# Performance work log

Hardware: AMD Instinct MI355X
Metric: run time of the kernel (lower is better)

Reference implementation:

```python
import jax, jax.numpy as jnp
import numpy as np

B = 32768; NF = 8; E = 16; V = 100000; D = 4
IN = 2 * NF * E          # 256 = id_dims + agn_dims
FCN = [256, 128, 64]
DIMS = [IN] + FCN
EPS = 1e-5               # BatchNorm1d eps


def setup_inputs() -> dict:
    ks = jax.random.split(jax.random.key(0), 64)
    inp = {
        'id_idx': jax.random.randint(ks[0], (B, NF), 0, V),
        'agn_idx': jax.random.randint(ks[1], (B, NF), 0, V),
        'domain_id': jax.random.randint(ks[2], (B,), 0, D),
        'id_tables': jax.random.normal(ks[3], (NF, V, E), dtype=jnp.float32) * 0.01,
        'agn_tables': jax.random.normal(ks[4], (NF, V, E), dtype=jnp.float32) * 0.01,
    }
    k = 5
    for i in range(len(FCN)):
        din, dout = DIMS[i], DIMS[i + 1]
        inp[f'mlp_W{i}'] = jax.random.normal(ks[k], (D, din, dout), dtype=jnp.float32) / np.sqrt(din).astype(np.float32); k += 1
        inp[f'mlp_b{i}'] = jnp.zeros((D, dout), jnp.float32)
        inp[f'bn_g{i}'] = jnp.ones((D, dout), jnp.float32)
        inp[f'bn_b{i}'] = jnp.zeros((D, dout), jnp.float32)
        inp[f'gate_W1_{i}'] = jax.random.normal(ks[k], (D, IN, dout), dtype=jnp.float32) / np.sqrt(IN).astype(np.float32); k += 1
        inp[f'gate_b1_{i}'] = jnp.zeros((D, dout), jnp.float32)
        inp[f'gate_W2_{i}'] = jax.random.normal(ks[k], (D, dout, dout), dtype=jnp.float32) / np.sqrt(dout).astype(np.float32); k += 1
        inp[f'gate_b2_{i}'] = jnp.zeros((D, dout), jnp.float32)
    inp['fin_W'] = jax.random.normal(ks[k], (D, DIMS[-1], 1), dtype=jnp.float32) / np.sqrt(DIMS[-1]).astype(np.float32)
    inp['fin_b'] = jnp.zeros((D, 1), jnp.float32)
    return inp


def _embed(tables, idx):
    # tables [NF,V,E], idx [B,NF] -> [B, NF*E] (per-feature lookup then concat)
    g = tables[jnp.arange(NF)[None, :], idx]            # [B,NF,E]
    return g.reshape(idx.shape[0], NF * E)


def _ppnet(id_tables, agn_tables, mlp_W, mlp_b, bn_g, bn_b, gW1, gb1, gW2, gb2,
           fin_W, fin_b, id_idx, agn_idx, domain_id):
    id_x = _embed(id_tables, id_idx)                    # [B, 128]
    agn_x = _embed(agn_tables, agn_idx)                 # [B, 128]
    # gate_input = cat(id_x, agn_x.detach())
    gate_in = jnp.concatenate([id_x, jax.lax.stop_gradient(agn_x)], axis=1)  # [B, IN]
    h = None
    for i in range(len(FCN)):
        # GateNU: Linear->ReLU->Linear->2*sigmoid, broadcast over D domain towers
        g1 = jax.nn.relu(jnp.einsum('bi,dio->dbo', gate_in, gW1[i]) + gb1[i][:, None, :])
        gate = 2.0 * jax.nn.sigmoid(jnp.einsum('dbo,dop->dbp', g1, gW2[i]) + gb2[i][:, None, :])
        # MLP layer: Linear -> BatchNorm1d (train-mode batch stats) -> ReLU
        if h is None:
            h = jnp.einsum('bi,dio->dbo', gate_in, mlp_W[i]) + mlp_b[i][:, None, :]
        else:
            h = jnp.einsum('dbi,dio->dbo', h, mlp_W[i]) + mlp_b[i][:, None, :]
        mu = h.mean(axis=1, keepdims=True)
        var = h.var(axis=1, keepdims=True)              # biased, matches torch BN training
        h = (h - mu) * jax.lax.rsqrt(var + EPS) * bn_g[i][:, None, :] + bn_b[i][:, None, :]
        h = jax.nn.relu(h)
        h = h * gate
    out = jax.nn.sigmoid(jnp.einsum('dbh,dho->dbo', h, fin_W) + fin_b[:, None, :])  # [D,B,1]
    out = out[:, :, 0]                                  # [D,B]
    # torch.where masked-select chain == gather the row of the assigned domain
    return out[domain_id, jnp.arange(out.shape[1])]     # [B]


def reference(id_idx, agn_idx, domain_id, id_tables, agn_tables,
              mlp_W0, mlp_b0, bn_g0, bn_b0, gate_W1_0, gate_b1_0, gate_W2_0, gate_b2_0,
              mlp_W1, mlp_b1, bn_g1, bn_b1, gate_W1_1, gate_b1_1, gate_W2_1, gate_b2_1,
              mlp_W2, mlp_b2, bn_g2, bn_b2, gate_W1_2, gate_b1_2, gate_W2_2, gate_b2_2,
              fin_W, fin_b):
    mlp_W = [mlp_W0, mlp_W1, mlp_W2]; mlp_b = [mlp_b0, mlp_b1, mlp_b2]
    bn_g = [bn_g0, bn_g1, bn_g2]; bn_b = [bn_b0, bn_b1, bn_b2]
    gW1 = [gate_W1_0, gate_W1_1, gate_W1_2]; gb1 = [gate_b1_0, gate_b1_1, gate_b1_2]
    gW2 = [gate_W2_0, gate_W2_1, gate_W2_2]; gb2 = [gate_b2_0, gate_b2_1, gate_b2_2]
    return _ppnet(id_tables, agn_tables, mlp_W, mlp_b, bn_g, bn_b, gW1, gb1, gW2, gb2,
                  fin_W, fin_b, id_idx, agn_idx, domain_id)
```

## Files before the change

kernel.cpp:

```cpp
#include <hip/hip_runtime.h>


typedef __attribute__((ext_vector_type(8))) short short8;
typedef __attribute__((ext_vector_type(4))) float floatx4;

#define BATCH 32768
#define NDOM 4
#define TM 128
#define TN 64
#define KSTEP 32
#define LDA 40

__device__ __forceinline__ unsigned short f2b(float f) {
    unsigned u = __float_as_uint(f);
    u += 0x7fffu + ((u >> 16) & 1u);
    return (unsigned short)(u >> 16);
}
__device__ __forceinline__ float b2f(unsigned short h) {
    return __uint_as_float(((unsigned)h) << 16);
}

struct MatDesc { const float* src; unsigned K, N, pfx, total; };
struct PrepArgs { MatDesc m[9]; float* stats; unsigned statsN; unsigned grand; };

__global__ __launch_bounds__(256) void prep_k(PrepArgs a, unsigned short* __restrict__ wt) {
    unsigned e = blockIdx.x * 256 + threadIdx.x;
    if (e < a.statsN) a.stats[e] = 0.f;
    if (e >= a.grand) return;
    int j = 0;
    while (j < 8 && e >= a.m[j].pfx + a.m[j].total) j++;
    const unsigned K = a.m[j].K, N = a.m[j].N;
    const unsigned local = e - a.m[j].pfx;
    const unsigned kn = K * N;
    const unsigned d = local / kn;
    const unsigned r2 = local - d * kn;
    const unsigned n = r2 / K;
    const unsigned k = r2 - n * K;
    wt[e] = f2b(a.m[j].src[((long long)d * K + k) * N + n]);
}

__global__ __launch_bounds__(256) void embed_k(const int* __restrict__ idi, const int* __restrict__ agi,
                                               const float* __restrict__ idt, const float* __restrict__ agt,
                                               unsigned short* __restrict__ gin) {
    int t = blockIdx.x * 256 + threadIdx.x;
    int b = t >> 4, slot = t & 15;
    int f = slot & 7;
    const int* ip = (slot < 8) ? idi : agi;
    const float* tab = (slot < 8) ? idt : agt;
    int ix = ip[b * 8 + f];
    const float* src = tab + ((long long)f * 100000 + ix) * 16;
    unsigned short tmp[16];
#pragma unroll
    for (int j = 0; j < 16; j++) tmp[j] = f2b(src[j]);
    unsigned short* dst = gin + (long long)b * 256 + slot * 16;
    *(uint4*)dst = *(const uint4*)tmp;
    *(uint4*)(dst + 8) = *(const uint4*)(tmp + 8);
}

__global__ __launch_bounds__(256) void gemm_ep(
    const unsigned short* __restrict__ X, long long xds,
    const unsigned short* __restrict__ Wt,
    const float* __restrict__ bias,
    void* outv,
    int N, int K, int mode, int hf32,
    const void* hprev,
    const float* __restrict__ muv, const float* __restrict__ rsv,
    const float* __restrict__ gma, const float* __restrict__ bta,
    float* __restrict__ gsum, float* __restrict__ gssq) {
    __shared__ __align__(16) unsigned short sA[TM * LDA];
    __shared__ __align__(16) unsigned short sB[TN * LDA];
    __shared__ float sSum[TN], sSsq[TN];

    const int t = threadIdx.x;
    const int d = blockIdx.z;
    const int m0 = blockIdx.x * TM, n0 = blockIdx.y * TN;
    const unsigned short* Xp = X + (long long)d * xds + (long long)m0 * K;
    const unsigned short* Wp = Wt + ((long long)d * N + n0) * (long long)K;

    floatx4 acc[2][4];
#pragma unroll
    for (int i = 0; i < 2; i++)
#pragma unroll
        for (int j = 0; j < 4; j++) acc[i][j] = (floatx4)(0.0f);

    const int w = t >> 6, lane = t & 63, lrow = lane & 15, lq = lane >> 4;
    const int arow = t >> 2, ach = t & 3;

    for (int k0 = 0; k0 < K; k0 += KSTEP) {
        *(uint4*)&sA[arow * LDA + ach * 8] = *(const uint4*)&Xp[(long long)arow * K + k0 + ach * 8];
        *(uint4*)&sA[(arow + 64) * LDA + ach * 8] = *(const uint4*)&Xp[(long long)(arow + 64) * K + k0 + ach * 8];
        *(uint4*)&sB[arow * LDA + ach * 8] = *(const uint4*)&Wp[(long long)arow * K + k0 + ach * 8];
        __syncthreads();
        short8 a[2], b[4];
#pragma unroll
        for (int rt = 0; rt < 2; rt++)
            a[rt] = *(const short8*)&sA[(w * 32 + rt * 16 + lrow) * LDA + lq * 8];
#pragma unroll
        for (int ct = 0; ct < 4; ct++)
            b[ct] = *(const short8*)&sB[(ct * 16 + lrow) * LDA + lq * 8];
#pragma unroll
        for (int rt = 0; rt < 2; rt++)
#pragma unroll
            for (int ct = 0; ct < 4; ct++)
                acc[rt][ct] = __builtin_amdgcn_mfma_f32_16x16x32_bf16(a[rt], b[ct], acc[rt][ct], 0, 0, 0);
        __syncthreads();
    }

    if (mode == 0) {
        if (t < TN) { sSum[t] = 0.f; sSsq[t] = 0.f; }
        __syncthreads();
    }

    const long long orow = (long long)d * BATCH + m0;
#pragma unroll
    for (int ct = 0; ct < 4; ct++) {
        const int nl = ct * 16 + lrow;
        const int n = n0 + nl;
        const float bs = bias[d * N + n];
        float mu_ = 0.f, sc_ = 0.f, bb_ = 0.f;
        if (mode == 2) {
            mu_ = muv[d * N + n];
            sc_ = rsv[d * N + n] * gma[d * N + n];
            bb_ = bta[d * N + n];
        }
        float s = 0.f, ss = 0.f;
#pragma unroll
        for (int rt = 0; rt < 2; rt++) {
            const int mb = w * 32 + rt * 16 + lq * 4;
#pragma unroll
            for (int r = 0; r < 4; r++) {
                float v = acc[rt][ct][r] + bs;
                const long long oi = (orow + mb + r) * (long long)N + n;
                if (mode == 0) {
                    s += v; ss += v * v;
                    if (hf32) ((float*)outv)[oi] = v;
                    else ((unsigned short*)outv)[oi] = f2b(v);
                } else if (mode == 1) {
                    v = fmaxf(v, 0.f);
                    ((unsigned short*)outv)[oi] = f2b(v);
                } else {
                    const float gate = 2.f / (1.f + __expf(-v));
                    const float h = hf32 ? ((const float*)hprev)[oi] : b2f(((const unsigned short*)hprev)[oi]);
                    float x = (h - mu_) * sc_ + bb_;
                    x = fmaxf(x, 0.f);
                    ((unsigned short*)outv)[oi] = f2b(x * gate);
                }
            }
        }
        if (mode == 0) {
            s += __shfl_down(s, 32); ss += __shfl_down(ss, 32);
            s += __shfl_down(s, 16); ss += __shfl_down(ss, 16);
            if (lane < 16) {
                atomicAdd(&sSum[nl], s);
                atomicAdd(&sSsq[nl], ss);
            }
        }
    }
    if (mode == 0) {
        __syncthreads();
        if (t < TN) {
            atomicAdd(&gsum[d * N + n0 + t], sSum[t]);
            atomicAdd(&gssq[d * N + n0 + t], sSsq[t]);
        }
    }
}

__global__ void bn_finalize(const float* __restrict__ gsum, const float* __restrict__ gssq,
                            float* __restrict__ muv, float* __restrict__ rsv, int total, float invB) {
    int i = blockIdx.x * blockDim.x + threadIdx.x;
    if (i >= total) return;
    float mu = gsum[i] * invB;
    float var = gssq[i] * invB - mu * mu;
    muv[i] = mu;
    rsv[i] = rsqrtf(var + 1e-5f);
}

__global__ __launch_bounds__(256) void final_k(const unsigned short* __restrict__ X3, const int* __restrict__ dom,
                                               const float* __restrict__ fw, const float* __restrict__ fb,
                                               float* __restrict__ out) {
    int b = blockIdx.x * 256 + threadIdx.x;
    int d = dom[b];
    const unsigned short* x = X3 + ((long long)d * BATCH + b) * 64;
    const float* wp = fw + d * 64;
    float acc = fb[d];
#pragma unroll
    for (int k = 0; k < 64; k++) acc += b2f(x[k]) * wp[k];
    out[b] = 1.f / (1.f + __expf(-acc));
}

extern "C" void kernel_launch(void* const* d_in, const int* in_sizes, int n_in,
                              void* d_out, int out_size, void* d_ws, size_t ws_size,
                              hipStream_t stream) {
    const int B = BATCH, D = NDOM;
    const int dims[4] = {256, 256, 128, 64};

    const int* id_idx = (const int*)d_in[0];
    const int* agn_idx = (const int*)d_in[1];
    const int* dom = (const int*)d_in[2];
    const float* id_t = (const float*)d_in[3];
    const float* agn_t = (const float*)d_in[4];
    const float *mlpW[3], *mlpb[3], *bng[3], *bnb[3], *gW1[3], *gb1[3], *gW2[3], *gb2[3];
    for (int i = 0; i < 3; i++) {
        int b0 = 5 + i * 8;
        mlpW[i] = (const float*)d_in[b0 + 0];
        mlpb[i] = (const float*)d_in[b0 + 1];
        bng[i]  = (const float*)d_in[b0 + 2];
        bnb[i]  = (const float*)d_in[b0 + 3];
        gW1[i]  = (const float*)d_in[b0 + 4];
        gb1[i]  = (const float*)d_in[b0 + 5];
        gW2[i]  = (const float*)d_in[b0 + 6];
        gb2[i]  = (const float*)d_in[b0 + 7];
    }
    const float* finW = (const float*)d_in[29];
    const float* finb = (const float*)d_in[30];

    char* wsc = (char*)d_ws;
    size_t off = 0;
    auto alloc = [&](size_t bytes) -> char* {
        char* p = wsc + off;
        off = (off + bytes + 255) & ~(size_t)255;
        return p;
    };

    struct { const float* src; int K, N; } mats[9] = {
        {mlpW[0], 256, 256}, {gW1[0], 256, 256}, {gW2[0], 256, 256},
        {mlpW[1], 256, 128}, {gW1[1], 256, 128}, {gW2[1], 128, 128},
        {mlpW[2], 128, 64},  {gW1[2], 256, 64},  {gW2[2], 64, 64}};
    unsigned pfx[10];
    pfx[0] = 0;
    for (int j = 0; j < 9; j++) pfx[j + 1] = pfx[j] + 4u * mats[j].K * mats[j].N;

    unsigned short* wt = (unsigned short*)alloc((size_t)pfx[9] * 2);
    unsigned short* gin = (unsigned short*)alloc((size_t)B * 256 * 2);
    float* stats = (float*)alloc((size_t)3 * 2 * D * 256 * 4);
    float* murs  = (float*)alloc((size_t)3 * 2 * D * 256 * 4);
    unsigned short* G = (unsigned short*)alloc((size_t)D * B * 256 * 2);

    size_t need32 = (size_t)D * B * 256 * 4 + (size_t)D * B * 128 * 4 +
                    (size_t)D * B * 256 * 2 + (size_t)D * B * 128 * 2 + 4096;
    int hf32 = (ws_size > off) && ((ws_size - off) >= need32);

    char *H0, *H1;
    unsigned short *Xb0, *Xb1;
    if (hf32) {
        H0 = alloc((size_t)D * B * 256 * 4);
        H1 = alloc((size_t)D * B * 128 * 4);
        Xb0 = (unsigned short*)alloc((size_t)D * B * 256 * 2);
        Xb1 = (unsigned short*)alloc((size_t)D * B * 128 * 2);
    } else {
        H0 = alloc((size_t)D * B * 256 * 2);
        H1 = alloc((size_t)D * B * 128 * 2);
        Xb0 = (unsigned short*)H0;
        Xb1 = (unsigned short*)H1;
    }

    PrepArgs pa;
    for (int j = 0; j < 9; j++) {
        pa.m[j].src = mats[j].src;
        pa.m[j].K = (unsigned)mats[j].K;
        pa.m[j].N = (unsigned)mats[j].N;
        pa.m[j].pfx = pfx[j];
        pa.m[j].total = 4u * mats[j].K * mats[j].N;
    }
    pa.stats = stats;
    pa.statsN = 3 * 2 * D * 256;
    pa.grand = pfx[9];

    prep_k<<<dim3((pfx[9] + 255) / 256), dim3(256), 0, stream>>>(pa, wt);
    embed_k<<<dim3(B * 16 / 256), dim3(256), 0, stream>>>(id_idx, agn_idx, id_t, agn_t, gin);

    const unsigned short* Xcur = gin;
    long long xds = 0;
    char* Hbuf[3] = {H0, H1, H0};
    unsigned short* Xout[3] = {Xb0, Xb1, Xb0};

    for (int i = 0; i < 3; i++) {
        const int K = dims[i], N = dims[i + 1];
        float* gsum_i = stats + (size_t)i * 2 * D * 256;
        float* gssq_i = gsum_i + D * 256;
        float* mu_i = murs + (size_t)i * 2 * D * 256;
        float* rs_i = mu_i + D * 256;
        unsigned short* wtM  = wt + pfx[i * 3 + 0];
        unsigned short* wtG1 = wt + pfx[i * 3 + 1];
        unsigned short* wtG2 = wt + pfx[i * 3 + 2];
        dim3 grid(B / TM, N / TN, D);

        gemm_ep<<<grid, 256, 0, stream>>>(Xcur, xds, wtM, mlpb[i], (void*)Hbuf[i],
                                          N, K, 0, hf32, nullptr, nullptr, nullptr, nullptr, nullptr,
                                          gsum_i, gssq_i);
        bn_finalize<<<(D * N + 255) / 256, 256, 0, stream>>>(gsum_i, gssq_i, mu_i, rs_i, D * N, 1.f / B);
        gemm_ep<<<grid, 256, 0, stream>>>(gin, 0, wtG1, gb1[i], (void*)G,
                                          N, 256, 1, 0, nullptr, nullptr, nullptr, nullptr, nullptr,
                                          nullptr, nullptr);
        gemm_ep<<<grid, 256, 0, stream>>>(G, (long long)B * N, wtG2, gb2[i], (void*)Xout[i],
                                          N, N, 2, hf32, (const void*)Hbuf[i], mu_i, rs_i, bng[i], bnb[i],
                                          nullptr, nullptr);
        Xcur = Xout[i];
        xds = (long long)B * N;
    }

    final_k<<<dim3(B / 256), dim3(256), 0, stream>>>(Xout[2], dom, finW, finb, (float*)d_out);
}
```

Baseline: 560.1 us.

## Fuse gate MLP, BN-normalize and gating per layer; recompute MLP GEMM after stats pass

Replaces the per-layer three-GEMM pipeline with a stats-only GEMM pass that accumulates BatchNorm sums without writing H, followed by one fused kernel. The fused kernel computes both gate GEMMs through shared memory, recomputes the MLP GEMM, applies folded BN scale/shift, ReLU and the gate, and writes only the next activation. The last layer also folds in the final projection and sigmoid, with a domain mask. It drops the H and G intermediate round trips and the mlp bias (which BN cancels), at the cost of doing the MLP GEMM twice and reading B fragments directly from global memory.

```diff
diff --git a/kernel.cpp b/kernel.cpp
--- a/kernel.cpp
+++ b/kernel.cpp
@@ -6,10 +6,7 @@
 
 #define BATCH 32768
 #define NDOM 4
-#define TM 128
-#define TN 64
-#define KSTEP 32
-#define LDA 40
+#define TM 64
 
 __device__ __forceinline__ unsigned short f2b(float f) {
     unsigned u = __float_as_uint(f);
@@ -57,159 +54,281 @@
     *(uint4*)(dst + 8) = *(const uint4*)(tmp + 8);
 }
 
-__global__ __launch_bounds__(256) void gemm_ep(
-    const unsigned short* __restrict__ X, long long xds,
-    const unsigned short* __restrict__ Wt,
-    const float* __restrict__ bias,
-    void* outv,
-    int N, int K, int mode, int hf32,
-    const void* hprev,
-    const float* __restrict__ muv, const float* __restrict__ rsv,
-    const float* __restrict__ gma, const float* __restrict__ bta,
+template <int N, int KX>
+__global__ __launch_bounds__(256, 2) void stats_k(
+    const unsigned short* __restrict__ X, int ginMode,
+    const unsigned short* __restrict__ Wm,
     float* __restrict__ gsum, float* __restrict__ gssq) {
-    __shared__ __align__(16) unsigned short sA[TM * LDA];
-    __shared__ __align__(16) unsigned short sB[TN * LDA];
-    __shared__ float sSum[TN], sSsq[TN];
-
+    constexpr int GX = KX / 8;
+    constexpr int NW = N / 4, CT = NW / 16;
+    __shared__ __align__(16) unsigned short tA[TM * KX];
     const int t = threadIdx.x;
-    const int d = blockIdx.z;
-    const int m0 = blockIdx.x * TM, n0 = blockIdx.y * TN;
-    const unsigned short* Xp = X + (long long)d * xds + (long long)m0 * K;
-    const unsigned short* Wp = Wt + ((long long)d * N + n0) * (long long)K;
-
-    floatx4 acc[2][4];
-#pragma unroll
-    for (int i = 0; i < 2; i++)
-#pragma unroll
-        for (int j = 0; j < 4; j++) acc[i][j] = (floatx4)(0.0f);
-
+    const int d = blockIdx.y;
+    const int m0 = blockIdx.x * TM;
+    const unsigned short* Xp = X + ((long long)(ginMode ? 0 : d * BATCH) + m0) * KX;
+#pragma unroll
+    for (int r = 0; r < TM * GX / 256; r++) {
+        int idx = r * 256 + t;
+        int m = idx / GX, j = idx % GX;
+        uint4 v = *(const uint4*)(Xp + (long long)m * KX + j * 8);
+        *(uint4*)&tA[(m * GX + (j ^ (m & 7))) * 8] = v;
+    }
+    __syncthreads();
     const int w = t >> 6, lane = t & 63, lrow = lane & 15, lq = lane >> 4;
-    const int arow = t >> 2, ach = t & 3;
-
-    for (int k0 = 0; k0 < K; k0 += KSTEP) {
-        *(uint4*)&sA[arow * LDA + ach * 8] = *(const uint4*)&Xp[(long long)arow * K + k0 + ach * 8];
-        *(uint4*)&sA[(arow + 64) * LDA + ach * 8] = *(const uint4*)&Xp[(long long)(arow + 64) * K + k0 + ach * 8];
-        *(uint4*)&sB[arow * LDA + ach * 8] = *(const uint4*)&Wp[(long long)arow * K + k0 + ach * 8];
-        __syncthreads();
-        short8 a[2], b[4];
-#pragma unroll
-        for (int rt = 0; rt < 2; rt++)
-            a[rt] = *(const short8*)&sA[(w * 32 + rt * 16 + lrow) * LDA + lq * 8];
-#pragma unroll
-        for (int ct = 0; ct < 4; ct++)
-            b[ct] = *(const short8*)&sB[(ct * 16 + lrow) * LDA + lq * 8];
-#pragma unroll
-        for (int rt = 0; rt < 2; rt++)
-#pragma unroll
-            for (int ct = 0; ct < 4; ct++)
+    const int n0w = w * NW;
+    const unsigned short* Wp = Wm + ((long long)d * N + n0w) * KX;
+    floatx4 acc[4][CT];
+#pragma unroll
+    for (int rt = 0; rt < 4; rt++)
+#pragma unroll
+        for (int ct = 0; ct < CT; ct++) acc[rt][ct] = (floatx4)(0.f);
+#pragma unroll
+    for (int k0 = 0; k0 < KX; k0 += 32) {
+        short8 a[4], b[CT];
+#pragma unroll
+        for (int rt = 0; rt < 4; rt++) {
+            int m = rt * 16 + lrow;
+            a[rt] = *(const short8*)&tA[(m * GX + (((k0 >> 3) | lq) ^ (m & 7))) * 8];
+        }
+#pragma unroll
+        for (int ct = 0; ct < CT; ct++)
+            b[ct] = *(const short8*)(Wp + (long long)(ct * 16 + lrow) * KX + k0 + lq * 8);
+#pragma unroll
+        for (int rt = 0; rt < 4; rt++)
+#pragma unroll
+            for (int ct = 0; ct < CT; ct++)
                 acc[rt][ct] = __builtin_amdgcn_mfma_f32_16x16x32_bf16(a[rt], b[ct], acc[rt][ct], 0, 0, 0);
-        __syncthreads();
-    }
-
-    if (mode == 0) {
-        if (t < TN) { sSum[t] = 0.f; sSsq[t] = 0.f; }
-        __syncthreads();
-    }
-
-    const long long orow = (long long)d * BATCH + m0;
-#pragma unroll
-    for (int ct = 0; ct < 4; ct++) {
-        const int nl = ct * 16 + lrow;
-        const int n = n0 + nl;
-        const float bs = bias[d * N + n];
-        float mu_ = 0.f, sc_ = 0.f, bb_ = 0.f;
-        if (mode == 2) {
-            mu_ = muv[d * N + n];
-            sc_ = rsv[d * N + n] * gma[d * N + n];
-            bb_ = bta[d * N + n];
-        }
+    }
+#pragma unroll
+    for (int ct = 0; ct < CT; ct++) {
         float s = 0.f, ss = 0.f;
 #pragma unroll
-        for (int rt = 0; rt < 2; rt++) {
-            const int mb = w * 32 + rt * 16 + lq * 4;
-#pragma unroll
-            for (int r = 0; r < 4; r++) {
-                float v = acc[rt][ct][r] + bs;
-                const long long oi = (orow + mb + r) * (long long)N + n;
-                if (mode == 0) {
-                    s += v; ss += v * v;
-                    if (hf32) ((float*)outv)[oi] = v;
-                    else ((unsigned short*)outv)[oi] = f2b(v);
-                } else if (mode == 1) {
-                    v = fmaxf(v, 0.f);
-                    ((unsigned short*)outv)[oi] = f2b(v);
-                } else {
-                    const float gate = 2.f / (1.f + __expf(-v));
-                    const float h = hf32 ? ((const float*)hprev)[oi] : b2f(((const unsigned short*)hprev)[oi]);
-                    float x = (h - mu_) * sc_ + bb_;
-                    x = fmaxf(x, 0.f);
-                    ((unsigned short*)outv)[oi] = f2b(x * gate);
-                }
-            }
-        }
-        if (mode == 0) {
-            s += __shfl_down(s, 32); ss += __shfl_down(ss, 32);
-            s += __shfl_down(s, 16); ss += __shfl_down(ss, 16);
-            if (lane < 16) {
-                atomicAdd(&sSum[nl], s);
-                atomicAdd(&sSsq[nl], ss);
-            }
-        }
-    }
-    if (mode == 0) {
-        __syncthreads();
-        if (t < TN) {
-            atomicAdd(&gsum[d * N + n0 + t], sSum[t]);
-            atomicAdd(&gssq[d * N + n0 + t], sSsq[t]);
-        }
-    }
-}
-
-__global__ void bn_finalize(const float* __restrict__ gsum, const float* __restrict__ gssq,
-                            float* __restrict__ muv, float* __restrict__ rsv, int total, float invB) {
+        for (int rt = 0; rt < 4; rt++)
+#pragma unroll
+            for (int r = 0; r < 4; r++) { float v = acc[rt][ct][r]; s += v; ss += v * v; }
+        s += __shfl_down(s, 32); ss += __shfl_down(ss, 32);
+        s += __shfl_down(s, 16); ss += __shfl_down(ss, 16);
+        if (lane < 16) {
+            atomicAdd(&gsum[d * N + n0w + ct * 16 + lane], s);
+            atomicAdd(&gssq[d * N + n0w + ct * 16 + lane], ss);
+        }
+    }
+}
+
+__global__ void fin_k(const float* __restrict__ gsum, const float* __restrict__ gssq,
+                      const float* __restrict__ gma, const float* __restrict__ bta,
+                      float* __restrict__ SC, float* __restrict__ SH, int total, float invB) {
     int i = blockIdx.x * blockDim.x + threadIdx.x;
     if (i >= total) return;
-    float mu = gsum[i] * invB;
-    float var = gssq[i] * invB - mu * mu;
-    muv[i] = mu;
-    rsv[i] = rsqrtf(var + 1e-5f);
-}
-
-__global__ __launch_bounds__(256) void final_k(const unsigned short* __restrict__ X3, const int* __restrict__ dom,
-                                               const float* __restrict__ fw, const float* __restrict__ fb,
-                                               float* __restrict__ out) {
-    int b = blockIdx.x * 256 + threadIdx.x;
-    int d = dom[b];
-    const unsigned short* x = X3 + ((long long)d * BATCH + b) * 64;
-    const float* wp = fw + d * 64;
-    float acc = fb[d];
-#pragma unroll
-    for (int k = 0; k < 64; k++) acc += b2f(x[k]) * wp[k];
-    out[b] = 1.f / (1.f + __expf(-acc));
+    float ma = gsum[i] * invB;
+    float var = gssq[i] * invB - ma * ma;
+    float rs = rsqrtf(var + 1e-5f);
+    float sc = rs * gma[i];
+    SC[i] = sc;
+    SH[i] = bta[i] - ma * sc;
+}
+
+template <int N, int KX, bool RESTAGE, bool FINAL>
+__global__ __launch_bounds__(256, 2) void fused_k(
+    const unsigned short* __restrict__ gin,
+    const unsigned short* __restrict__ Xh,
+    const unsigned short* __restrict__ W1,
+    const unsigned short* __restrict__ W2,
+    const unsigned short* __restrict__ Wm,
+    const float* __restrict__ gb1, const float* __restrict__ gb2,
+    const float* __restrict__ SC, const float* __restrict__ SH,
+    unsigned short* __restrict__ Xn,
+    const int* __restrict__ dom, const float* __restrict__ fw,
+    const float* __restrict__ fb, float* __restrict__ outp) {
+    constexpr int GG = N / 8;
+    constexpr int GX = KX / 8;
+    constexpr int NW = N / 4, CT = NW / 16;
+    __shared__ __align__(16) unsigned short tA[TM * 256];
+    __shared__ __align__(16) unsigned short g1b[TM * N];
+    const int t = threadIdx.x;
+    const int d = blockIdx.y;
+    const int m0 = blockIdx.x * TM;
+    const int w = t >> 6, lane = t & 63, lrow = lane & 15, lq = lane >> 4;
+    const int n0w = w * NW;
+
+    {
+        const unsigned short* Gp = gin + (long long)m0 * 256;
+#pragma unroll
+        for (int r = 0; r < 8; r++) {
+            int idx = r * 256 + t;
+            int m = idx >> 5, j = idx & 31;
+            uint4 v = *(const uint4*)(Gp + (long long)m * 256 + j * 8);
+            *(uint4*)&tA[((m << 5) + (j ^ (m & 7))) * 8] = v;
+        }
+    }
+    __syncthreads();
+
+    floatx4 acc1[4][CT];
+#pragma unroll
+    for (int rt = 0; rt < 4; rt++)
+#pragma unroll
+        for (int ct = 0; ct < CT; ct++) acc1[rt][ct] = (floatx4)(0.f);
+    const unsigned short* W1p = W1 + ((long long)d * N + n0w) * 256;
+#pragma unroll
+    for (int k0 = 0; k0 < 256; k0 += 32) {
+        short8 a[4], b[CT];
+#pragma unroll
+        for (int rt = 0; rt < 4; rt++) {
+            int m = rt * 16 + lrow;
+            a[rt] = *(const short8*)&tA[((m << 5) + (((k0 >> 3) | lq) ^ (m & 7))) * 8];
+        }
+#pragma unroll
+        for (int ct = 0; ct < CT; ct++)
+            b[ct] = *(const short8*)(W1p + (long long)(ct * 16 + lrow) * 256 + k0 + lq * 8);
+#pragma unroll
+        for (int rt = 0; rt < 4; rt++)
+#pragma unroll
+            for (int ct = 0; ct < CT; ct++)
+                acc1[rt][ct] = __builtin_amdgcn_mfma_f32_16x16x32_bf16(a[rt], b[ct], acc1[rt][ct], 0, 0, 0);
+    }
+#pragma unroll
+    for (int ct = 0; ct < CT; ct++) {
+        int n = n0w + ct * 16 + lrow;
+        float bs = gb1[d * N + n];
+        int jj = n >> 3, sub = n & 7;
+#pragma unroll
+        for (int rt = 0; rt < 4; rt++)
+#pragma unroll
+            for (int r = 0; r < 4; r++) {
+                int m = rt * 16 + lq * 4 + r;
+                g1b[(m * GG + (jj ^ (m & 7))) * 8 + sub] = f2b(fmaxf(acc1[rt][ct][r] + bs, 0.f));
+            }
+    }
+    __syncthreads();
+
+    floatx4 acc2[4][CT];
+#pragma unroll
+    for (int rt = 0; rt < 4; rt++)
+#pragma unroll
+        for (int ct = 0; ct < CT; ct++) acc2[rt][ct] = (floatx4)(0.f);
+    const unsigned short* W2p = W2 + ((long long)d * N + n0w) * N;
+#pragma unroll
+    for (int k0 = 0; k0 < N; k0 += 32) {
+        short8 a[4], b[CT];
+#pragma unroll
+        for (int rt = 0; rt < 4; rt++) {
+            int m = rt * 16 + lrow;
+            a[rt] = *(const short8*)&g1b[(m * GG + (((k0 >> 3) | lq) ^ (m & 7))) * 8];
+        }
+#pragma unroll
+        for (int ct = 0; ct < CT; ct++)
+            b[ct] = *(const short8*)(W2p + (long long)(ct * 16 + lrow) * N + k0 + lq * 8);
+#pragma unroll
+        for (int rt = 0; rt < 4; rt++)
+#pragma unroll
+            for (int ct = 0; ct < CT; ct++)
+                acc2[rt][ct] = __builtin_amdgcn_mfma_f32_16x16x32_bf16(a[rt], b[ct], acc2[rt][ct], 0, 0, 0);
+    }
+    float gate[4][CT][4];
+#pragma unroll
+    for (int ct = 0; ct < CT; ct++) {
+        int n = n0w + ct * 16 + lrow;
+        float bs = gb2[d * N + n];
+#pragma unroll
+        for (int rt = 0; rt < 4; rt++)
+#pragma unroll
+            for (int r = 0; r < 4; r++)
+                gate[rt][ct][r] = 2.f / (1.f + __expf(-(acc2[rt][ct][r] + bs)));
+    }
+
+    if (RESTAGE) {
+        const unsigned short* Xp = Xh + ((long long)d * BATCH + m0) * KX;
+#pragma unroll
+        for (int r = 0; r < TM * GX / 256; r++) {
+            int idx = r * 256 + t;
+            int m = idx / GX, j = idx % GX;
+            uint4 v = *(const uint4*)(Xp + (long long)m * KX + j * 8);
+            *(uint4*)&tA[(m * GX + (j ^ (m & 7))) * 8] = v;
+        }
+    }
+    __syncthreads();
+
+    floatx4 acch[4][CT];
+#pragma unroll
+    for (int rt = 0; rt < 4; rt++)
+#pragma unroll
+        for (int ct = 0; ct < CT; ct++) acch[rt][ct] = (floatx4)(0.f);
+    const unsigned short* Wmp = Wm + ((long long)d * N + n0w) * KX;
+#pragma unroll
+    for (int k0 = 0; k0 < KX; k0 += 32) {
+        short8 a[4], b[CT];
+#pragma unroll
+        for (int rt = 0; rt < 4; rt++) {
+            int m = rt * 16 + lrow;
+            a[rt] = *(const short8*)&tA[(m * GX + (((k0 >> 3) | lq) ^ (m & 7))) * 8];
+        }
+#pragma unroll
+        for (int ct = 0; ct < CT; ct++)
+            b[ct] = *(const short8*)(Wmp + (long long)(ct * 16 + lrow) * KX + k0 + lq * 8);
+#pragma unroll
+        for (int rt = 0; rt < 4; rt++)
+#pragma unroll
+            for (int ct = 0; ct < CT; ct++)
+                acch[rt][ct] = __builtin_amdgcn_mfma_f32_16x16x32_bf16(a[rt], b[ct], acch[rt][ct], 0, 0, 0);
+    }
+#pragma unroll
+    for (int ct = 0; ct < CT; ct++) {
+        int n = n0w + ct * 16 + lrow;
+        float sc = SC[d * N + n], sh = SH[d * N + n];
+#pragma unroll
+        for (int rt = 0; rt < 4; rt++)
+#pragma unroll
+            for (int r = 0; r < 4; r++) {
+                int m = rt * 16 + lq * 4 + r;
+                float v = fmaxf(acch[rt][ct][r] * sc + sh, 0.f) * gate[rt][ct][r];
+                g1b[m * N + n] = f2b(v);
+            }
+    }
+    __syncthreads();
+
+    if (!FINAL) {
+        unsigned short* Op = Xn + ((long long)d * BATCH + m0) * N;
+#pragma unroll
+        for (int r = 0; r < TM * GG / 256; r++) {
+            int idx = r * 256 + t;
+            int m = idx / GG, j = idx % GG;
+            *(uint4*)(Op + (long long)m * N + j * 8) = *(const uint4*)&g1b[(m * GG + j) * 8];
+        }
+    } else {
+        int m = t >> 2, q = t & 3;
+        const float* fwp = fw + d * 64;
+        float s = 0.f;
+#pragma unroll
+        for (int k = 0; k < 16; k++) s += b2f(g1b[m * 64 + q * 16 + k]) * fwp[q * 16 + k];
+        s += __shfl_down(s, 1);
+        s += __shfl_down(s, 2);
+        if (q == 0) {
+            int b = m0 + m;
+            if (dom[b] == d) outp[b] = 1.f / (1.f + __expf(-(s + fb[d])));
+        }
+    }
 }
 
 extern "C" void kernel_launch(void* const* d_in, const int* in_sizes, int n_in,
                               void* d_out, int out_size, void* d_ws, size_t ws_size,
                               hipStream_t stream) {
     const int B = BATCH, D = NDOM;
-    const int dims[4] = {256, 256, 128, 64};
 
     const int* id_idx = (const int*)d_in[0];
     const int* agn_idx = (const int*)d_in[1];
     const int* dom = (const int*)d_in[2];
     const float* id_t = (const float*)d_in[3];
     const float* agn_t = (const float*)d_in[4];
-    const float *mlpW[3], *mlpb[3], *bng[3], *bnb[3], *gW1[3], *gb1[3], *gW2[3], *gb2[3];
+    const float *mlpW[3], *bng[3], *bnb[3], *gW1[3], *gb1[3], *gW2[3], *gb2[3];
     for (int i = 0; i < 3; i++) {
         int b0 = 5 + i * 8;
         mlpW[i] = (const float*)d_in[b0 + 0];
-        mlpb[i] = (const float*)d_in[b0 + 1];
-        bng[i]  = (const float*)d_in[b0 + 2];
-        bnb[i]  = (const float*)d_in[b0 + 3];
-        gW1[i]  = (const float*)d_in[b0 + 4];
-        gb1[i]  = (const float*)d_in[b0 + 5];
-        gW2[i]  = (const float*)d_in[b0 + 6];
-        gb2[i]  = (const float*)d_in[b0 + 7];
+        bng[i] = (const float*)d_in[b0 + 2];
+        bnb[i] = (const float*)d_in[b0 + 3];
+        gW1[i] = (const float*)d_in[b0 + 4];
+        gb1[i] = (const float*)d_in[b0 + 5];
+        gW2[i] = (const float*)d_in[b0 + 6];
+        gb2[i] = (const float*)d_in[b0 + 7];
     }
     const float* finW = (const float*)d_in[29];
     const float* finb = (const float*)d_in[30];
@@ -233,26 +352,9 @@
     unsigned short* wt = (unsigned short*)alloc((size_t)pfx[9] * 2);
     unsigned short* gin = (unsigned short*)alloc((size_t)B * 256 * 2);
     float* stats = (float*)alloc((size_t)3 * 2 * D * 256 * 4);
-    float* murs  = (float*)alloc((size_t)3 * 2 * D * 256 * 4);
-    unsigned short* G = (unsigned short*)alloc((size_t)D * B * 256 * 2);
-
-    size_t need32 = (size_t)D * B * 256 * 4 + (size_t)D * B * 128 * 4 +
-                    (size_t)D * B * 256 * 2 + (size_t)D * B * 128 * 2 + 4096;
-    int hf32 = (ws_size > off) && ((ws_size - off) >= need32);
-
-    char *H0, *H1;
-    unsigned short *Xb0, *Xb1;
-    if (hf32) {
-        H0 = alloc((size_t)D * B * 256 * 4);
-        H1 = alloc((size_t)D * B * 128 * 4);
-        Xb0 = (unsigned short*)alloc((size_t)D * B * 256 * 2);
-        Xb1 = (unsigned short*)alloc((size_t)D * B * 128 * 2);
-    } else {
-        H0 = alloc((size_t)D * B * 256 * 2);
-        H1 = alloc((size_t)D * B * 128 * 2);
-        Xb0 = (unsigned short*)H0;
-        Xb1 = (unsigned short*)H1;
-    }
+    float* scsh = (float*)alloc((size_t)3 * 2 * D * 256 * 4);
+    unsigned short* X1 = (unsigned short*)alloc((size_t)D * B * 256 * 2);
+    unsigned short* X2 = (unsigned short*)alloc((size_t)D * B * 128 * 2);
 
     PrepArgs pa;
     for (int j = 0; j < 9; j++) {
@@ -266,38 +368,34 @@
     pa.statsN = 3 * 2 * D * 256;
     pa.grand = pfx[9];
 
-    prep_k<<<dim3((pfx[9] + 255) / 256), dim3(256), 0, stream>>>(pa, wt);
-    embed_k<<<dim3(B * 16 / 256), dim3(256), 0, stream>>>(id_idx, agn_idx, id_t, agn_t, gin);
-
-    const unsigned short* Xcur = gin;
-    long long xds = 0;
-    char* Hbuf[3] = {H0, H1, H0};
-    unsigned short* Xout[3] = {Xb0, Xb1, Xb0};
-
-    for (int i = 0; i < 3; i++) {
-        const int K = dims[i], N = dims[i + 1];
-        float* gsum_i = stats + (size_t)i * 2 * D * 256;
-        float* gssq_i = gsum_i + D * 256;
-        float* mu_i = murs + (size_t)i * 2 * D * 256;
-        float* rs_i = mu_i + D * 256;
-        unsigned short* wtM  = wt + pfx[i * 3 + 0];
-        unsigned short* wtG1 = wt + pfx[i * 3 + 1];
-        unsigned short* wtG2 = wt + pfx[i * 3 + 2];
-        dim3 grid(B / TM, N / TN, D);
-
-        gemm_ep<<<grid, 256, 0, stream>>>(Xcur, xds, wtM, mlpb[i], (void*)Hbuf[i],
-                                          N, K, 0, hf32, nullptr, nullptr, nullptr, nullptr, nullptr,
-                                          gsum_i, gssq_i);
-        bn_finalize<<<(D * N + 255) / 256, 256, 0, stream>>>(gsum_i, gssq_i, mu_i, rs_i, D * N, 1.f / B);
-        gemm_ep<<<grid, 256, 0, stream>>>(gin, 0, wtG1, gb1[i], (void*)G,
-                                          N, 256, 1, 0, nullptr, nullptr, nullptr, nullptr, nullptr,
-                                          nullptr, nullptr);
-        gemm_ep<<<grid, 256, 0, stream>>>(G, (long long)B * N, wtG2, gb2[i], (void*)Xout[i],
-                                          N, N, 2, hf32, (const void*)Hbuf[i], mu_i, rs_i, bng[i], bnb[i],
-                                          nullptr, nullptr);
-        Xcur = Xout[i];
-        xds = (long long)B * N;
-    }
-
-    final_k<<<dim3(B / 256), dim3(256), 0, stream>>>(Xout[2], dom, finW, finb, (float*)d_out);
-}
+    const float invB = 1.f / (float)B;
+    dim3 gs(B / TM, D);
+
+    prep_k<<<dim3((pfx[9] + 255) / 256), 256, 0, stream>>>(pa, wt);
+    embed_k<<<dim3(B * 16 / 256), 256, 0, stream>>>(id_idx, agn_idx, id_t, agn_t, gin);
+
+    float* gsum0 = stats + 0 * 2 * D * 256; float* gssq0 = gsum0 + D * 256;
+    float* gsum1 = stats + 1 * 2 * D * 256; float* gssq1 = gsum1 + D * 256;
+    float* gsum2 = stats + 2 * 2 * D * 256; float* gssq2 = gsum2 + D * 256;
+    float* SC0 = scsh + 0 * 2 * D * 256; float* SH0 = SC0 + D * 256;
+    float* SC1 = scsh + 1 * 2 * D * 256; float* SH1 = SC1 + D * 256;
+    float* SC2 = scsh + 2 * 2 * D * 256; float* SH2 = SC2 + D * 256;
+
+    stats_k<256, 256><<<gs, 256, 0, stream>>>(gin, 1, wt + pfx[0], gsum0, gssq0);
+    fin_k<<<(D * 256 + 255) / 256, 256, 0, stream>>>(gsum0, gssq0, bng[0], bnb[0], SC0, SH0, D * 256, invB);
+    fused_k<256, 256, false, false><<<gs, 256, 0, stream>>>(
+        gin, gin, wt + pfx[1], wt + pfx[2], wt + pfx[0], gb1[0], gb2[0], SC0, SH0,
+        X1, nullptr, nullptr, nullptr, nullptr);
+
+    stats_k<128, 256><<<gs, 256, 0, stream>>>(X1, 0, wt + pfx[3], gsum1, gssq1);
+    fin_k<<<(D * 128 + 255) / 256, 256, 0, stream>>>(gsum1, gssq1, bng[1], bnb[1], SC1, SH1, D * 128, invB);
+    fused_k<128, 256, true, false><<<gs, 256, 0, stream>>>(
+        gin, X1, wt + pfx[4], wt + pfx[5], wt + pfx[3], gb1[1], gb2[1], SC1, SH1,
+        X2, nullptr, nullptr, nullptr, nullptr);
+
+    stats_k<64, 128><<<gs, 256, 0, stream>>>(X2, 0, wt + pfx[6], gsum2, gssq2);
+    fin_k<<<(D * 64 + 255) / 256, 256, 0, stream>>>(gsum2, gssq2, bng[2], bnb[2], SC2, SH2, D * 64, invB);
+    fused_k<64, 128, true, true><<<gs, 256, 0, stream>>>(
+        gin, X2, wt + pfx[7], wt + pfx[8], wt + pfx[6], gb1[2], gb2[2], SC2, SH2,
+        nullptr, dom, finW, finb, (float*)d_out);
+}
```

After: 506.7 us. -9.5%, faster.
